# Optimization experiments

Hardware: AMD Instinct MI355X
Metric: run time of the kernel (lower is better)

## Reference

```python
import jax, jax.numpy as jnp
import numpy as np

N_NODES = 50000
N_EDGES = 1600000
IN_CH = 128
OUT_CH = 64
HEADS = 2
NEG_SLOPE = 0.2


def setup_inputs() -> dict:
    key = jax.random.key(0)
    ks = jax.random.split(key, 9)
    return {
        "x": jax.random.normal(ks[0], (N_NODES, IN_CH), dtype=jnp.float32),
        "embedding": jax.random.normal(ks[1], (N_NODES, OUT_CH), dtype=jnp.float32),
        "lin_w": jax.random.normal(ks[2], (IN_CH, HEADS * OUT_CH), dtype=jnp.float32) * (1.0 / np.sqrt(IN_CH)),
        "att_i": jax.random.normal(ks[3], (HEADS, OUT_CH), dtype=jnp.float32) * 0.1,
        "att_j": jax.random.normal(ks[4], (HEADS, OUT_CH), dtype=jnp.float32) * 0.1,
        "att_em_i": jax.random.normal(ks[5], (HEADS, OUT_CH), dtype=jnp.float32) * 0.1,
        "att_em_j": jax.random.normal(ks[6], (HEADS, OUT_CH), dtype=jnp.float32) * 0.1,
        "edge_src": jax.random.randint(ks[7], (N_EDGES,), 0, N_NODES, dtype=jnp.int64 if jax.config.read("jax_enable_x64") else jnp.int32),
        "edge_dst": jax.random.randint(ks[8], (N_EDGES,), 0, N_NODES, dtype=jnp.int64 if jax.config.read("jax_enable_x64") else jnp.int32),
    }


def reference(x, embedding, lin_w, att_i, att_j, att_em_i, att_em_j, edge_src, edge_dst):
    N = x.shape[0]
    H, D = att_i.shape
    # linear projection: [N, H, D]
    xh = (x @ lin_w).reshape(N, H, D)
    # add self loops
    loop = jnp.arange(N, dtype=edge_src.dtype)
    src = jnp.concatenate([edge_src, loop])
    dst = jnp.concatenate([edge_dst, loop])
    # per-node attention scores (cat(x, emb) . cat(att, att_em) split into two dots)
    s_i = jnp.einsum("nhd,hd->nh", xh, att_i) + embedding @ att_em_i.T  # [N,H]
    s_j = jnp.einsum("nhd,hd->nh", xh, att_j) + embedding @ att_em_j.T  # [N,H]
    # per-edge attention: x_i is src feature, x_j is dst feature (as in source)
    alpha = jax.nn.leaky_relu(s_i[src] + s_j[dst], negative_slope=NEG_SLOPE)  # [E+N,H]
    alpha = jax.nn.softmax(alpha, axis=1)  # softmax over heads, per the source code
    # message is alpha * x[dst]; aggregated at dst => x[n] * sum of alpha over incoming edges
    w = jax.ops.segment_sum(alpha, dst, num_segments=N)  # [N,H]
    out = xh * w[:, :, None]  # [N,H,D]
    return out.mean(axis=1)  # [N,D]
```

## Files before the change

### kernel.cpp

```cpp
#include <hip/hip_runtime.h>
#include <hip/hip_bf16.h>

#define IN_CH 128
#define OUT_CH 64
#define NEG_SLOPE 0.2f
#define KPACK 1024.5f

#define BSHIFT 8
#define CHUNK 6250
#define NGEMM 256
#define CAPMAX 9216

typedef short bf16x8 __attribute__((ext_vector_type(8)));
typedef float f32x4 __attribute__((ext_vector_type(4)));
typedef unsigned long long u64;

__device__ __forceinline__ unsigned short f2bf(float f) {
  union { float f; unsigned u; } v;
  v.f = f;
  unsigned r = v.u + 0x7FFF + ((v.u >> 16) & 1);
  return (unsigned short)(r >> 16);
}

__global__ __launch_bounds__(256) void prep_kernel(
    const float* __restrict__ lw, const float* __restrict__ att_i,
    const float* __restrict__ att_j, float* __restrict__ u,
    int* __restrict__ gcur) {
  const int tid = threadIdx.x;
  const int which = blockIdx.x;
  if (which == 0) gcur[tid] = 0;
  const float* att = which ? att_j : att_i;
  int k = tid & 127;
  int h = (tid >> 7) & 1;
  float v = 0.f;
#pragma unroll 8
  for (int d = 0; d < 64; ++d)
    v = fmaf(lw[(size_t)k * IN_CH + h * 64 + d], att[h * 64 + d], v);
  u[which * 256 + h * 128 + k] = v;
}

__global__ __launch_bounds__(256) void score_kernel(
    const float* __restrict__ x, const float* __restrict__ emb,
    const float* __restrict__ u, const float* __restrict__ aei,
    const float* __restrict__ aej, float2* __restrict__ si,
    float2* __restrict__ sj, float* __restrict__ wself,
    float* __restrict__ wsum, int N) {
  const int tid = threadIdx.x;
  const int wave = tid >> 6;
  const int lane = tid & 63;
  const int n = blockIdx.x * 4 + wave;
  if (n >= N) return;

  float x0 = x[(size_t)n * IN_CH + lane];
  float x1 = x[(size_t)n * IN_CH + 64 + lane];
  float em = emb[(size_t)n * OUT_CH + lane];

  float v_si0 = fmaf(x0, u[lane], fmaf(x1, u[64 + lane], em * aei[lane]));
  float v_si1 =
      fmaf(x0, u[128 + lane], fmaf(x1, u[192 + lane], em * aei[64 + lane]));
  float v_sj0 =
      fmaf(x0, u[256 + lane], fmaf(x1, u[320 + lane], em * aej[lane]));
  float v_sj1 =
      fmaf(x0, u[384 + lane], fmaf(x1, u[448 + lane], em * aej[64 + lane]));

#pragma unroll
  for (int off = 32; off > 0; off >>= 1) {
    v_si0 += __shfl_xor(v_si0, off, 64);
    v_si1 += __shfl_xor(v_si1, off, 64);
    v_sj0 += __shfl_xor(v_sj0, off, 64);
    v_sj1 += __shfl_xor(v_sj1, off, 64);
  }

  if (lane == 0) {
    si[n] = make_float2(v_si0, v_si1);
    sj[n] = make_float2(v_sj0, v_sj1);
    float a0 = v_si0 + v_sj0;
    float a1 = v_si1 + v_sj1;
    a0 = a0 > 0.f ? a0 : NEG_SLOPE * a0;
    a1 = a1 > 0.f ? a1 : NEG_SLOPE * a1;
    wself[n] = 1.f / (1.f + __expf(a1 - a0));
    wsum[n] = 0.f;
  }
}

__global__ __launch_bounds__(256) void bin_gemm_kernel(
    const float* __restrict__ x, const float* __restrict__ lw,
    const int* __restrict__ esrc, const int* __restrict__ edst,
    const float2* __restrict__ si, const float2* __restrict__ sj,
    float* __restrict__ xh, float* __restrict__ wsum,
    u64* __restrict__ brecs, int* __restrict__ gcur, int cap, int nbin, int N,
    int E) {
  __shared__ __align__(16) u64 smem8[CHUNK];
  __shared__ int hist[256];
  __shared__ int scan[256];
  __shared__ int gbase[256];
  __shared__ int cur[256];
  const int bid = blockIdx.x;
  const int tid = threadIdx.x;
  const int wave = tid >> 6;
  const int lane = tid & 63;

  if (bid < nbin) {
    u64* recs = smem8;

    hist[tid] = 0;
    __syncthreads();

    const long e0 = (long)bid * CHUNK;
    const int cnt = (int)min((long)CHUNK, (long)E - e0);

    for (int r = tid; r < cnt; r += 256)
      atomicAdd(&hist[edst[e0 + r] >> BSHIFT], 1);
    __syncthreads();

    scan[tid] = hist[tid];
    __syncthreads();
#pragma unroll
    for (int ofs = 1; ofs < 256; ofs <<= 1) {
      int t = (tid >= ofs) ? scan[tid - ofs] : 0;
      __syncthreads();
      scan[tid] += t;
      __syncthreads();
    }
    int excl = scan[tid] - hist[tid];
    __syncthreads();
    scan[tid] = excl;
    cur[tid] = excl;
    gbase[tid] = (hist[tid] > 0) ? atomicAdd(&gcur[tid], hist[tid]) : 0;
    __syncthreads();

    for (int r = tid; r < cnt; r += 256) {
      long e = e0 + r;
      int s = esrc[e];
      int d = edst[e];
      float2 aa = si[s];
      float2 bb = sj[d];
      float a0 = aa.x + bb.x;
      float a1 = aa.y + bb.y;
      a0 = a0 > 0.f ? a0 : NEG_SLOPE * a0;
      a1 = a1 > 0.f ? a1 : NEG_SLOPE * a1;
      float p0 = 1.f / (1.f + __expf(a1 - a0));
      float val = KPACK + p0;
      int pos = atomicAdd(&cur[d >> BSHIFT], 1);
      recs[pos] = ((u64)(unsigned)d << 32) | (u64)__float_as_uint(val);
    }
    __syncthreads();

    for (int b = wave; b < 256; b += 4) {
      int c = hist[b];
      int s0 = scan[b];
      int g0 = gbase[b];
      u64* dp = brecs + (size_t)b * cap;
      for (int r = lane; r < c; r += 64) {
        u64 rec = recs[s0 + r];
        int gofs = g0 + r;
        if (gofs < cap) {
          dp[gofs] = rec;
        } else {
          unsafeAtomicAdd(&wsum[(int)(rec >> 32)],
                          __uint_as_float((unsigned)rec));
        }
      }
    }
  } else {
    typedef unsigned short BlRow[136];
    BlRow* Bl = (BlRow*)smem8;
    const int g = bid - nbin;

    for (int i = tid; i < IN_CH * IN_CH; i += 256) {
      int k = i >> 7;
      int c = i & 127;
      Bl[c][k] = f2bf(lw[i]);
    }
    __syncthreads();

    const int ntiles = (N + 63) / 64;
    const int ko = (lane >> 4) * 8;
    const int ccol = lane & 15;
    for (int tile = g; tile < ntiles; tile += NGEMM) {
      const int row0 = tile * 64 + wave * 16;
      int arow = row0 + (lane & 15);
      if (arow >= N) arow = N - 1;
      const float* ap = x + (size_t)arow * IN_CH + ko;
      bf16x8 a[4];
#pragma unroll
      for (int kb = 0; kb < 4; ++kb) {
        float4 f0 = *(const float4*)(ap + kb * 32);
        float4 f1 = *(const float4*)(ap + kb * 32 + 4);
        bf16x8 t;
        t[0] = (short)f2bf(f0.x); t[1] = (short)f2bf(f0.y);
        t[2] = (short)f2bf(f0.z); t[3] = (short)f2bf(f0.w);
        t[4] = (short)f2bf(f1.x); t[5] = (short)f2bf(f1.y);
        t[6] = (short)f2bf(f1.z); t[7] = (short)f2bf(f1.w);
        a[kb] = t;
      }
      const int crow0 = row0 + (lane >> 4) * 4;
#pragma unroll
      for (int nt = 0; nt < 8; ++nt) {
        f32x4 acc = {0.f, 0.f, 0.f, 0.f};
        const bf16x8* bp = (const bf16x8*)&Bl[nt * 16 + ccol][ko];
        acc = __builtin_amdgcn_mfma_f32_16x16x32_bf16(a[0], bp[0], acc, 0, 0, 0);
        acc = __builtin_amdgcn_mfma_f32_16x16x32_bf16(a[1], bp[4], acc, 0, 0, 0);
        acc = __builtin_amdgcn_mfma_f32_16x16x32_bf16(a[2], bp[8], acc, 0, 0, 0);
        acc = __builtin_amdgcn_mfma_f32_16x16x32_bf16(a[3], bp[12], acc, 0, 0, 0);
#pragma unroll
        for (int rr = 0; rr < 4; ++rr) {
          int n = crow0 + rr;
          if (n < N) xh[(size_t)n * IN_CH + nt * 16 + ccol] = acc[rr];
        }
      }
    }
  }
}

__global__ __launch_bounds__(1024) void reduce_out_kernel(
    const float* __restrict__ xh, const float* __restrict__ wsum,
    const float* __restrict__ wself, const u64* __restrict__ brecs,
    const int* __restrict__ gcur, int cap, float* __restrict__ out, int N) {
  __shared__ float table[256];
  const int b = blockIdx.x;
  const int tid = threadIdx.x;

  if (tid < 256) table[tid] = 0.f;
  __syncthreads();

  const int cnt = min(gcur[b], cap);
  const u64* rp = brecs + (size_t)b * cap;
  for (int r = tid; r < cnt; r += 1024) {
    u64 rec = rp[r];
    atomicAdd(&table[(int)(rec >> 32) & 255], __uint_as_float((unsigned)rec));
  }
  __syncthreads();
  const int n0 = b << BSHIFT;
  if (tid < 256 && n0 + tid < N) table[tid] += wsum[n0 + tid];
  __syncthreads();

  const int nmax = min(256, N - n0);
  for (int t = tid; t < nmax * 16; t += 1024) {
    int ln = t >> 4;
    int n = n0 + ln;
    int c4 = (t & 15) << 2;
    float wsv = table[ln];
    float cntf = floorf(wsv * (1.0f / KPACK));
    float s0 = wsv - KPACK * cntf;
    float p0s = wself[n];
    float w0 = s0 + p0s;
    float w1 = (cntf - s0) + (1.f - p0s);
    float4 v0 = *(const float4*)&xh[(size_t)n * IN_CH + c4];
    float4 v1 = *(const float4*)&xh[(size_t)n * IN_CH + 64 + c4];
    float4 o;
    o.x = 0.5f * fmaf(v0.x, w0, v1.x * w1);
    o.y = 0.5f * fmaf(v0.y, w0, v1.y * w1);
    o.z = 0.5f * fmaf(v0.z, w0, v1.z * w1);
    o.w = 0.5f * fmaf(v0.w, w0, v1.w * w1);
    *(float4*)&out[(size_t)n * OUT_CH + c4] = o;
  }
}

extern "C" void kernel_launch(void* const* d_in, const int* in_sizes, int n_in,
                              void* d_out, int out_size, void* d_ws,
                              size_t ws_size, hipStream_t stream) {
  const float* x = (const float*)d_in[0];
  const float* emb = (const float*)d_in[1];
  const float* lw = (const float*)d_in[2];
  const float* att_i = (const float*)d_in[3];
  const float* att_j = (const float*)d_in[4];
  const float* aei = (const float*)d_in[5];
  const float* aej = (const float*)d_in[6];
  const int* esrc = (const int*)d_in[7];
  const int* edst = (const int*)d_in[8];
  float* out = (float*)d_out;

  int N = in_sizes[0] / IN_CH;
  int E = in_sizes[7];
  int nb = (N + 255) >> BSHIFT;
  int nbin = (E + CHUNK - 1) / CHUNK;

  char* ws = (char*)d_ws;
  float* xh = (float*)ws;
  float2* si = (float2*)(ws + (size_t)N * IN_CH * 4);
  float2* sj = si + N;
  float* wself = (float*)(sj + N);
  float* wsum = wself + N;
  float* u = wsum + N;
  int* gcur = (int*)(u + 512);
  u64* brecs = (u64*)(gcur + 256);

  size_t fixed = (size_t)((char*)brecs - ws);
  size_t avail = ws_size > fixed ? (ws_size - fixed) / 8 : 0;
  int cap = (int)(avail / (nb > 0 ? nb : 1));
  if (cap > CAPMAX) cap = CAPMAX;
  if (cap < 1024) cap = 1024;

  prep_kernel<<<dim3(2), dim3(256), 0, stream>>>(lw, att_i, att_j, u, gcur);
  score_kernel<<<dim3((N + 3) / 4), dim3(256), 0, stream>>>(
      x, emb, u, aei, aej, si, sj, wself, wsum, N);
  bin_gemm_kernel<<<dim3(nbin + NGEMM), dim3(256), 0, stream>>>(
      x, lw, esrc, edst, si, sj, xh, wsum, brecs, gcur, cap, nbin, N, E);
  reduce_out_kernel<<<dim3(nb), dim3(1024), 0, stream>>>(
      xh, wsum, wself, brecs, gcur, cap, out, N);
}
```

Baseline: 171.1 us.

## Pack edge records into 32-bit fixed-point with u64 count/sum accumulation

Edge bin records shrink from 64-bit (full dst index plus packed float) to 32-bit (8-bit local node index plus 20-bit fixed-point probability). This halves global record write and read traffic and shared memory per chunk, which allows a larger CHUNK. The reduce kernel accumulates an integer count and a fixed-point sum in one u64 shared atomic instead of the float KPACK trick, which avoids precision loss from large packed sums. It adds quantization error of about 1e-6 per edge and needs 64-bit LDS atomics.

```diff
diff --git a/kernel.cpp b/kernel.cpp
--- a/kernel.cpp
+++ b/kernel.cpp
@@ -7,13 +7,15 @@
 #define KPACK 1024.5f
 
 #define BSHIFT 8
-#define CHUNK 6250
+#define CHUNK 8192
 #define NGEMM 256
 #define CAPMAX 9216
+#define FIX20 1048576.0f
 
 typedef short bf16x8 __attribute__((ext_vector_type(8)));
 typedef float f32x4 __attribute__((ext_vector_type(4)));
 typedef unsigned long long u64;
+typedef unsigned int u32;
 
 __device__ __forceinline__ unsigned short f2bf(float f) {
   union { float f; unsigned u; } v;
@@ -88,9 +90,9 @@
     const int* __restrict__ esrc, const int* __restrict__ edst,
     const float2* __restrict__ si, const float2* __restrict__ sj,
     float* __restrict__ xh, float* __restrict__ wsum,
-    u64* __restrict__ brecs, int* __restrict__ gcur, int cap, int nbin, int N,
+    u32* __restrict__ brecs, int* __restrict__ gcur, int cap, int nbin, int N,
     int E) {
-  __shared__ __align__(16) u64 smem8[CHUNK];
+  __shared__ __align__(16) u64 smem8[4352];
   __shared__ int hist[256];
   __shared__ int scan[256];
   __shared__ int gbase[256];
@@ -101,7 +103,7 @@
   const int lane = tid & 63;
 
   if (bid < nbin) {
-    u64* recs = smem8;
+    u32* recs = (u32*)smem8;
 
     hist[tid] = 0;
     __syncthreads();
@@ -140,9 +142,9 @@
       a0 = a0 > 0.f ? a0 : NEG_SLOPE * a0;
       a1 = a1 > 0.f ? a1 : NEG_SLOPE * a1;
       float p0 = 1.f / (1.f + __expf(a1 - a0));
-      float val = KPACK + p0;
+      u32 fx = (u32)fminf(p0 * FIX20 + 0.5f, 1048575.0f);
       int pos = atomicAdd(&cur[d >> BSHIFT], 1);
-      recs[pos] = ((u64)(unsigned)d << 32) | (u64)__float_as_uint(val);
+      recs[pos] = ((u32)(d & 255) << 20) | fx;
     }
     __syncthreads();
 
@@ -150,15 +152,16 @@
       int c = hist[b];
       int s0 = scan[b];
       int g0 = gbase[b];
-      u64* dp = brecs + (size_t)b * cap;
+      u32* dp = brecs + (size_t)b * cap;
+      int base = (b << BSHIFT) & ~255;
       for (int r = lane; r < c; r += 64) {
-        u64 rec = recs[s0 + r];
+        u32 rec = recs[s0 + r];
         int gofs = g0 + r;
         if (gofs < cap) {
           dp[gofs] = rec;
         } else {
-          unsafeAtomicAdd(&wsum[(int)(rec >> 32)],
-                          __uint_as_float((unsigned)rec));
+          float p0 = (float)(rec & 0xFFFFF) * (1.0f / FIX20);
+          unsafeAtomicAdd(&wsum[base + (int)(rec >> 20)], KPACK + p0);
         }
       }
     }
@@ -215,37 +218,38 @@
 
 __global__ __launch_bounds__(1024) void reduce_out_kernel(
     const float* __restrict__ xh, const float* __restrict__ wsum,
-    const float* __restrict__ wself, const u64* __restrict__ brecs,
+    const float* __restrict__ wself, const u32* __restrict__ brecs,
     const int* __restrict__ gcur, int cap, float* __restrict__ out, int N) {
-  __shared__ float table[256];
+  __shared__ u64 table[256];
   const int b = blockIdx.x;
   const int tid = threadIdx.x;
 
-  if (tid < 256) table[tid] = 0.f;
+  if (tid < 256) table[tid] = 0ull;
   __syncthreads();
 
   const int cnt = min(gcur[b], cap);
-  const u64* rp = brecs + (size_t)b * cap;
+  const u32* rp = brecs + (size_t)b * cap;
   for (int r = tid; r < cnt; r += 1024) {
-    u64 rec = rp[r];
-    atomicAdd(&table[(int)(rec >> 32) & 255], __uint_as_float((unsigned)rec));
+    u32 rec = rp[r];
+    atomicAdd(&table[rec >> 20], (1ull << 32) | (u64)(rec & 0xFFFFF));
   }
   __syncthreads();
+
   const int n0 = b << BSHIFT;
-  if (tid < 256 && n0 + tid < N) table[tid] += wsum[n0 + tid];
-  __syncthreads();
-
   const int nmax = min(256, N - n0);
   for (int t = tid; t < nmax * 16; t += 1024) {
     int ln = t >> 4;
     int n = n0 + ln;
     int c4 = (t & 15) << 2;
-    float wsv = table[ln];
-    float cntf = floorf(wsv * (1.0f / KPACK));
-    float s0 = wsv - KPACK * cntf;
+    u64 acc = table[ln];
+    float cnt_i = (float)(u32)(acc >> 32);
+    float s0_i = (float)(u32)(acc & 0xFFFFFFFFu) * (1.0f / FIX20);
+    float wsv = wsum[n];
+    float cnt_s = floorf(wsv * (1.0f / KPACK));
+    float s0_s = wsv - KPACK * cnt_s;
     float p0s = wself[n];
-    float w0 = s0 + p0s;
-    float w1 = (cntf - s0) + (1.f - p0s);
+    float w0 = s0_i + s0_s + p0s;
+    float w1 = (cnt_i + cnt_s - s0_i - s0_s) + (1.f - p0s);
     float4 v0 = *(const float4*)&xh[(size_t)n * IN_CH + c4];
     float4 v1 = *(const float4*)&xh[(size_t)n * IN_CH + 64 + c4];
     float4 o;
@@ -284,10 +288,10 @@
   float* wsum = wself + N;
   float* u = wsum + N;
   int* gcur = (int*)(u + 512);
-  u64* brecs = (u64*)(gcur + 256);
+  u32* brecs = (u32*)(gcur + 256);
 
   size_t fixed = (size_t)((char*)brecs - ws);
-  size_t avail = ws_size > fixed ? (ws_size - fixed) / 8 : 0;
+  size_t avail = ws_size > fixed ? (ws_size - fixed) / 4 : 0;
   int cap = (int)(avail / (nb > 0 ? nb : 1));
   if (cap > CAPMAX) cap = CAPMAX;
   if (cap < 1024) cap = 1024;
```

Measured after the change: 167.0 us. 2.4% less time.
